# Kernel tuning notes

Measured on AMD Instinct MI355X. Metric: run time of the kernel, lower is better.

Reference implementation:

```python
import jax, jax.numpy as jnp
import numpy as np

B = 8192          # tokens
H = 7168          # hidden size
E = 256           # routed experts
N_GROUP = 8
GROUP_SIZE = 32   # E // N_GROUP
TOPK_GROUP = 4
TOPK = 8
SCALE = 2.5
EPS = 1e-20
NEG_INF = -jnp.inf


def setup_inputs() -> dict:
    key = jax.random.key(0)
    k1, k2, k3 = jax.random.split(key, 3)
    x = jax.random.normal(k1, (1, 1, B, H), dtype=jnp.float32)
    weight = jax.random.normal(k2, (H, E), dtype=jnp.float32) * 0.02
    bias = jax.random.uniform(k3, (E,), dtype=jnp.float32)  # e_score_correction_bias
    return {"x": x, "weight": weight, "bias": bias}


def reference(x, weight, bias):
    # gate projection + softmax over experts
    logits = jnp.einsum('abth,he->abte', x, weight)          # [1,1,B,E]
    scores = jax.nn.softmax(logits, axis=-1)                 # [1,1,B,E]
    scores_with_bias = scores + bias                         # bias-corrected scores

    # group-limited routing: top-2 per group, summed -> group score
    grouped = scores_with_bias.reshape(1, 1, B, N_GROUP, GROUP_SIZE)
    top2_vals, _ = jax.lax.top_k(grouped, 2)                 # [1,1,B,8,2]
    group_scores = top2_vals.sum(axis=-1)                    # [1,1,B,8]

    # select top-4 groups, build {1, -inf} mask over groups
    _, top4_idx = jax.lax.top_k(group_scores, TOPK_GROUP)    # [1,1,B,4]
    sel = jax.nn.one_hot(top4_idx, N_GROUP, dtype=scores.dtype).sum(axis=-2)  # [1,1,B,8]
    group_mask = jnp.where(sel > 0, 1.0, NEG_INF)
    expert_mask = jnp.repeat(group_mask, GROUP_SIZE, axis=-1)  # [1,1,B,256]

    # mask (multiplicative, as in original), top-8 experts
    masked = scores_with_bias * expert_mask
    _, top8_idx = jax.lax.top_k(masked, TOPK)                # [1,1,B,8]

    # gather unbiased scores, normalize, eps + scale
    w = jnp.take_along_axis(scores, top8_idx, axis=-1)       # [1,1,B,8]
    w = w / w.sum(axis=-1, keepdims=True)
    w = (w + EPS) * SCALE
    return w, top8_idx
```

## Files before the change

### kernel.cpp

```cpp
#include <hip/hip_runtime.h>
#include <math.h>

#define B_TOK 8192
#define H_DIM 7168
#define E_NUM 256
#define NKS   4
#define KSL   (H_DIM / NKS)
#define BK    32
#define NSTEP (KSL / BK)
#define BM    128
#define NMT   (B_TOK / BM)
#define FLAG_CAP 512
#define TAU   2e-6

typedef _Float16 f16;
typedef __attribute__((ext_vector_type(8))) _Float16 f16x8;
typedef __attribute__((ext_vector_type(4))) float    f32x4;

typedef __attribute__((address_space(1))) const void gvoid_t;
typedef __attribute__((address_space(3))) void       lvoid_t;

__device__ inline void gload_lds16(const void* g, void* s) {
    __builtin_amdgcn_global_load_lds((gvoid_t*)g, (lvoid_t*)s, 16, 0, 0);
}

__device__ __forceinline__ void route_token(
    const double* lv, const double* bj, int l, int hf, int t,
    float* __restrict__ out, double* ming_adj, double* ming_grp)
{
    double m = fmax(fmax(lv[0], lv[1]), fmax(lv[2], lv[3]));
    #pragma unroll
    for (int d = 1; d < 64; d <<= 1) m = fmax(m, __shfl_xor(m, d, 64));
    double sc[4], zs = 0.0;
    #pragma unroll
    for (int q = 0; q < 4; ++q) { sc[q] = exp(lv[q] - m); zs += sc[q]; }
    #pragma unroll
    for (int d = 1; d < 64; d <<= 1) zs += __shfl_xor(zs, d, 64);
    double swb[4];
    #pragma unroll
    for (int q = 0; q < 4; ++q) { sc[q] /= zs; swb[q] = sc[q] + bj[q]; }

    double gsq[4];
    #pragma unroll
    for (int q = 0; q < 4; ++q) {
        double a = swb[q], b = -INFINITY;
        #pragma unroll
        for (int d = 1; d <= 16; d <<= 1) {
            double oa = __shfl_xor(a, d, 64), ob = __shfl_xor(b, d, 64);
            double na = fmax(a, oa);
            double nb = fmax(fmin(a, oa), fmax(b, ob));
            a = na; b = nb;
        }
        gsq[q] = a + b;
    }
    double gsv[8];
    #pragma unroll
    for (int q = 0; q < 4; ++q) {
        gsv[2 * q]     = __shfl(gsq[q], 0, 64);
        gsv[2 * q + 1] = __shfl(gsq[q], 32, 64);
    }

    unsigned selmask = 0; double g4 = 0.0, g5 = 0.0;
    #pragma unroll
    for (int k = 0; k < 5; ++k) {
        double best = -INFINITY; int bg = 0;
        #pragma unroll
        for (int g = 0; g < 8; ++g)
            if (gsv[g] > best) { best = gsv[g]; bg = g; }
        if (k < 4) { selmask |= 1u << bg; g4 = best; } else g5 = best;
        #pragma unroll
        for (int g = 0; g < 8; ++g) if (g == bg) gsv[g] = -INFINITY;
    }
    *ming_grp = g4 - g5;

    double mk[4];
    #pragma unroll
    for (int q = 0; q < 4; ++q)
        mk[q] = ((selmask >> (2 * q + hf)) & 1u) ? swb[q] : -INFINITY;

    double wk[8]; int ek[8]; double wsum = 0.0;
    double prev = 0.0, ming = 1e300;
    #pragma unroll
    for (int k = 0; k < 9; ++k) {
        double vbest = mk[0]; int ebest = l;
        #pragma unroll
        for (int q = 1; q < 4; ++q)
            if (mk[q] > vbest) { vbest = mk[q]; ebest = l + 64 * q; }
        #pragma unroll
        for (int d = 1; d < 64; d <<= 1) {
            double ov = __shfl_xor(vbest, d, 64);
            int    oe = __shfl_xor(ebest, d, 64);
            if (ov > vbest || (ov == vbest && oe < ebest)) { vbest = ov; ebest = oe; }
        }
        if (k > 0) ming = fmin(ming, prev - vbest);
        prev = vbest;
        if (k < 8) {
            const int ol = ebest & 63, oq = ebest >> 6;
            if (l == ol) {
                #pragma unroll
                for (int q = 0; q < 4; ++q) if (q == oq) mk[q] = -INFINITY;
            }
            double cand = (oq == 0) ? sc[0] : (oq == 1) ? sc[1] : (oq == 2) ? sc[2] : sc[3];
            double sv = __shfl(cand, ol, 64);
            wk[k] = sv; ek[k] = ebest; wsum += sv;
        }
    }
    *ming_adj = ming;

    if (l == 0) {
        const double inv = 1.0 / wsum;
        #pragma unroll
        for (int k = 0; k < 8; ++k) {
            out[(size_t)t * 8 + k] = (float)((wk[k] * inv + 1e-20) * 2.5);
            out[(size_t)B_TOK * 8 + (size_t)t * 8 + k] = (float)ek[k];
        }
    }
}

__global__ void convert_w_kernel(const float* __restrict__ W,
                                 f16* __restrict__ wpk,
                                 unsigned* __restrict__ flags) {
    if (blockIdx.x == 0 && threadIdx.x == 0) flags[0] = 0;
    int g = blockIdx.x * 256 + threadIdx.x;
    int n = g & 255, k = g >> 8;
    float v = W[(size_t)k * E_NUM + n];
    f16 hi = (f16)v;
    f16 lo = (f16)(v - (float)hi);
    int kf = k >> 5, tq = (k >> 3) & 3, j = k & 7;
    int nf = n >> 4, l = tq * 16 + (n & 15);
    size_t off = ((size_t)(kf * 16 + nf) * 2) * 512 + (size_t)l * 8 + j;
    wpk[off]       = hi;
    wpk[off + 512] = lo;
}

__global__ __launch_bounds__(512, 1)
void gemm_kernel(const float* __restrict__ x,
                 const f16* __restrict__ wpk,
                 float* __restrict__ partial) {
    __shared__ __align__(16) char lds[2][49152];

    const int tid = threadIdx.x;
    const int l   = tid & 63;
    const int wid = tid >> 6;
    const int mt  = blockIdx.x >> 2;
    const int ks  = blockIdx.x & 3;
    const int wr  = wid >> 2;
    const int wc  = wid & 3;

    const int row = mt * BM + wid * 16 + (l & 15);
    const float* xrow = x + (size_t)row * H_DIM + ks * KSL + (l >> 4) * 8;

    f32x4 acc[4][4];
    #pragma unroll
    for (int mi = 0; mi < 4; ++mi)
        #pragma unroll
        for (int ni = 0; ni < 4; ++ni) acc[mi][ni] = (f32x4)0.0f;

    {
        float4 a0 = *reinterpret_cast<const float4*>(xrow);
        float4 a1 = *reinterpret_cast<const float4*>(xrow + 4);
        const int kf = ks * NSTEP + 0;
        #pragma unroll
        for (int i = 0; i < 4; ++i) {
            int fi = wid * 4 + i, nf = fi >> 1, h = fi & 1;
            const f16* src = wpk + ((size_t)(kf * 16 + nf) * 2 + h) * 512 + (size_t)l * 8;
            gload_lds16(src, &lds[0][16384 + (nf * 2 + h) * 1024]);
        }
        float fv[8] = {a0.x, a0.y, a0.z, a0.w, a1.x, a1.y, a1.z, a1.w};
        f16x8 hv, lo;
        #pragma unroll
        for (int j = 0; j < 8; ++j) {
            f16 hh = (f16)fv[j];
            hv[j] = hh;
            lo[j] = (f16)(fv[j] - (float)hh);
        }
        *reinterpret_cast<f16x8*>(&lds[0][(wid * 2 + 0) * 1024 + l * 16]) = hv;
        *reinterpret_cast<f16x8*>(&lds[0][(wid * 2 + 1) * 1024 + l * 16]) = lo;
        __syncthreads();
    }

    int cur = 0;
    for (int s = 0; s < NSTEP; ++s) {
        const bool hn = (s + 1) < NSTEP;
        const int  sn = hn ? s + 1 : s;

        float4 a0 = *reinterpret_cast<const float4*>(xrow + (size_t)sn * BK);
        float4 a1 = *reinterpret_cast<const float4*>(xrow + (size_t)sn * BK + 4);

        if (hn) {
            const int kf = ks * NSTEP + sn;
            char* nb = lds[cur ^ 1];
            #pragma unroll
            for (int i = 0; i < 4; ++i) {
                int fi = wid * 4 + i, nf = fi >> 1, h = fi & 1;
                const f16* src = wpk + ((size_t)(kf * 16 + nf) * 2 + h) * 512 + (size_t)l * 8;
                gload_lds16(src, &nb[16384 + (nf * 2 + h) * 1024]);
            }
        }

        const char* Ab = lds[cur];
        const char* Bb = lds[cur] + 16384;
        f16x8 af[4][2], bf[4][2];
        #pragma unroll
        for (int mi = 0; mi < 4; ++mi)
            #pragma unroll
            for (int h = 0; h < 2; ++h)
                af[mi][h] = *reinterpret_cast<const f16x8*>(
                    Ab + ((wr * 4 + mi) * 2 + h) * 1024 + l * 16);
        #pragma unroll
        for (int ni = 0; ni < 4; ++ni)
            #pragma unroll
            for (int h = 0; h < 2; ++h)
                bf[ni][h] = *reinterpret_cast<const f16x8*>(
                    Bb + ((wc * 4 + ni) * 2 + h) * 1024 + l * 16);
        #pragma unroll
        for (int mi = 0; mi < 4; ++mi)
            #pragma unroll
            for (int ni = 0; ni < 4; ++ni) {
                acc[mi][ni] = __builtin_amdgcn_mfma_f32_16x16x32_f16(
                    af[mi][0], bf[ni][0], acc[mi][ni], 0, 0, 0);
                acc[mi][ni] = __builtin_amdgcn_mfma_f32_16x16x32_f16(
                    af[mi][0], bf[ni][1], acc[mi][ni], 0, 0, 0);
                acc[mi][ni] = __builtin_amdgcn_mfma_f32_16x16x32_f16(
                    af[mi][1], bf[ni][0], acc[mi][ni], 0, 0, 0);
            }

        if (hn) {
            char* nb = lds[cur ^ 1];
            float fv[8] = {a0.x, a0.y, a0.z, a0.w, a1.x, a1.y, a1.z, a1.w};
            f16x8 hv, lo;
            #pragma unroll
            for (int j = 0; j < 8; ++j) {
                f16 hh = (f16)fv[j];
                hv[j] = hh;
                lo[j] = (f16)(fv[j] - (float)hh);
            }
            *reinterpret_cast<f16x8*>(&nb[(wid * 2 + 0) * 1024 + l * 16]) = hv;
            *reinterpret_cast<f16x8*>(&nb[(wid * 2 + 1) * 1024 + l * 16]) = lo;
        }
        __syncthreads();
        cur ^= 1;
    }

    float* pbase = partial + ((size_t)ks * B_TOK + (size_t)mt * BM) * E_NUM;
    #pragma unroll
    for (int mi = 0; mi < 4; ++mi)
        #pragma unroll
        for (int ni = 0; ni < 4; ++ni)
            #pragma unroll
            for (int r = 0; r < 4; ++r) {
                int rr = wr * 64 + mi * 16 + (l >> 4) * 4 + r;
                int cc = wc * 64 + ni * 16 + (l & 15);
                pbase[(size_t)rr * E_NUM + cc] = acc[mi][ni][r];
            }
}

__global__ __launch_bounds__(512, 1)
void routing_kernel(const float* __restrict__ partial,
                    const float* __restrict__ bias,
                    float* __restrict__ out,
                    unsigned* __restrict__ flags) {
    const int tid  = threadIdx.x;
    const int l    = tid & 63;
    const int wv   = tid >> 6;
    const int tok0 = blockIdx.x * 32;

    double bj[4];
    #pragma unroll
    for (int q = 0; q < 4; ++q) bj[q] = (double)bias[l + 64 * q];
    const int hf = l >> 5;

    for (int i = 0; i < 4; ++i) {
        const int t = tok0 + wv * 4 + i;
        double lv[4];
        #pragma unroll
        for (int q = 0; q < 4; ++q) {
            double s = 0.0;
            #pragma unroll
            for (int ksl = 0; ksl < NKS; ++ksl)
                s += (double)partial[((size_t)ksl * B_TOK + t) * E_NUM + l + 64 * q];
            lv[q] = s;
        }
        double ma, mg;
        route_token(lv, bj, l, hf, t, out, &ma, &mg);
        if (l == 0 && (ma < TAU || mg < TAU)) {
            unsigned idx = atomicAdd(&flags[0], 1u);
            if (idx < FLAG_CAP) flags[1 + idx] = (unsigned)t;
        }
    }
}

__global__ __launch_bounds__(256)
void recompute_dot_kernel(const float* __restrict__ x,
                          const float* __restrict__ W,
                          const unsigned* __restrict__ flags,
                          double* __restrict__ dpart) {
    __shared__ float xs[896];
    unsigned count = flags[0]; if (count > FLAG_CAP) count = FLAG_CAP;
    unsigned nj = count * 8;
    for (unsigned j = blockIdx.x; j < nj; j += gridDim.x) {
        unsigned li = j >> 3, sl = j & 7;
        int t = (int)flags[1 + li];
        const float* xb = x + (size_t)t * H_DIM + sl * 896;
        for (int i = threadIdx.x; i < 224; i += 256)
            *reinterpret_cast<float4*>(&xs[i * 4]) =
                *reinterpret_cast<const float4*>(xb + i * 4);
        __syncthreads();
        const float* wp = W + (size_t)(sl * 896) * E_NUM + threadIdx.x;
        double acc = 0.0;
        #pragma unroll 8
        for (int k = 0; k < 896; ++k)
            acc += (double)xs[k] * (double)wp[(size_t)k * E_NUM];
        dpart[((size_t)li * 8 + sl) * E_NUM + threadIdx.x] = acc;
        __syncthreads();
    }
}

__global__ __launch_bounds__(64)
void recompute_route_kernel(const double* __restrict__ dpart,
                            const float* __restrict__ bias,
                            const unsigned* __restrict__ flags,
                            float* __restrict__ out) {
    const int l = threadIdx.x;
    unsigned count = flags[0]; if (count > FLAG_CAP) count = FLAG_CAP;
    double bj[4];
    #pragma unroll
    for (int q = 0; q < 4; ++q) bj[q] = (double)bias[l + 64 * q];
    const int hf = l >> 5;
    for (unsigned li = blockIdx.x; li < count; li += gridDim.x) {
        int t = (int)flags[1 + li];
        double lv[4];
        #pragma unroll
        for (int q = 0; q < 4; ++q) {
            double s = 0.0;
            #pragma unroll
            for (int sl = 0; sl < 8; ++sl)
                s += dpart[((size_t)li * 8 + sl) * E_NUM + l + 64 * q];
            lv[q] = s;
        }
        double ma, mg;
        route_token(lv, bj, l, hf, t, out, &ma, &mg);
    }
}

#define TM 32
#define HB 64
#define FNST (H_DIM / HB)

__global__ __launch_bounds__(512, 1)
void moe_gate_fallback(const float* __restrict__ x,
                       const float* __restrict__ W,
                       const float* __restrict__ bias,
                       float* __restrict__ out) {
    __shared__ double xs[TM][HB];
    const int tid  = threadIdx.x;
    const int l    = tid & 63;
    const int wv   = tid >> 6;
    const int tok0 = blockIdx.x * TM;
    const int tl = tid >> 4;
    const int ho = (tid & 15) * 4;

    double acc[4][4];
    #pragma unroll
    for (int i = 0; i < 4; ++i)
        #pragma unroll
        for (int q = 0; q < 4; ++q) acc[i][q] = 0.0;

    const float* xrow = x + (size_t)(tok0 + tl) * H_DIM + ho;
    float4 v = *reinterpret_cast<const float4*>(xrow);

    for (int s = 0; s < FNST; ++s) {
        __syncthreads();
        xs[tl][ho + 0] = (double)v.x;
        xs[tl][ho + 1] = (double)v.y;
        xs[tl][ho + 2] = (double)v.z;
        xs[tl][ho + 3] = (double)v.w;
        __syncthreads();
        const int sn = (s + 1 < FNST) ? s + 1 : s;
        v = *reinterpret_cast<const float4*>(xrow + (size_t)sn * HB);
        const float* wh = W + (size_t)s * HB * E_NUM + l;
        #pragma unroll 4
        for (int h = 0; h < HB; h += 2) {
            float wf0[4], wf1[4];
            #pragma unroll
            for (int q = 0; q < 4; ++q) {
                wf0[q] = wh[(size_t)h       * E_NUM + q * 64];
                wf1[q] = wh[(size_t)(h + 1) * E_NUM + q * 64];
            }
            #pragma unroll
            for (int i = 0; i < 4; ++i) {
                const double2 xv = *reinterpret_cast<const double2*>(&xs[wv * 4 + i][h]);
                #pragma unroll
                for (int q = 0; q < 4; ++q) {
                    acc[i][q] = fma((double)wf0[q], xv.x, acc[i][q]);
                    acc[i][q] = fma((double)wf1[q], xv.y, acc[i][q]);
                }
            }
        }
    }

    double bj[4];
    #pragma unroll
    for (int q = 0; q < 4; ++q) bj[q] = (double)bias[l + 64 * q];
    const int hf = l >> 5;

    for (int i = 0; i < 4; ++i) {
        const int t = tok0 + wv * 4 + i;
        double lv[4];
        #pragma unroll
        for (int q = 0; q < 4; ++q) lv[q] = acc[i][q];
        double ma, mg;
        route_token(lv, bj, l, hf, t, out, &ma, &mg);
    }
}

extern "C" void kernel_launch(void* const* d_in, const int* in_sizes, int n_in,
                              void* d_out, int out_size, void* d_ws, size_t ws_size,
                              hipStream_t stream) {
    const float* x    = (const float*)d_in[0];
    const float* W    = (const float*)d_in[1];
    const float* bias = (const float*)d_in[2];
    float* out = (float*)d_out;

    const size_t flag_off = 7864320;
    const size_t part_off = 8u * 1024 * 1024;
    const size_t need     = part_off + (size_t)NKS * B_TOK * E_NUM * 4;

    if (ws_size >= need) {
        f16*      wpk     = (f16*)d_ws;
        unsigned* flags   = (unsigned*)((char*)d_ws + flag_off);
        float*    partial = (float*)((char*)d_ws + part_off);
        double*   dpart   = (double*)((char*)d_ws + part_off);

        convert_w_kernel<<<(H_DIM * E_NUM) / 256, 256, 0, stream>>>(W, wpk, flags);
        gemm_kernel<<<NMT * NKS, 512, 0, stream>>>(x, wpk, partial);
        routing_kernel<<<B_TOK / 32, 512, 0, stream>>>(partial, bias, out, flags);
        recompute_dot_kernel<<<1024, 256, 0, stream>>>(x, W, flags, dpart);
        recompute_route_kernel<<<64, 64, 0, stream>>>(dpart, bias, flags, out);
    } else {
        moe_gate_fallback<<<B_TOK / 32, 512, 0, stream>>>(x, W, bias, out);
    }
}
```

Baseline: 216.4 us.

## Triple-buffer GEMM LDS with explicit waitcnt pipeline, block swizzle, and MFMA priority

Moves the gate GEMM from a double-buffered LDS loop to a three-buffer pipeline, unrolled by two steps. Weight tiles are staged two steps ahead and x loads are prefetched into registers, with explicit vmcnt/lgkmcnt waits and raw s_barrier in place of __syncthreads. The block index is swizzled so that concurrently running blocks share the same K-slice, and s_setprio raises wave priority around the MFMA section. The cost is 144KB of LDS per block, plus waitcnt counts that depend on the exact number of outstanding loads, which is fragile.

After: 213.1 us. No clear change (-1.5%).

```diff
diff --git a/kernel.cpp b/kernel.cpp
--- a/kernel.cpp
+++ b/kernel.cpp
@@ -23,6 +23,11 @@
 __device__ inline void gload_lds16(const void* g, void* s) {
     __builtin_amdgcn_global_load_lds((gvoid_t*)g, (lvoid_t*)s, 16, 0, 0);
 }
+
+#define WAITVM(N) do { asm volatile("s_waitcnt vmcnt(" #N ")" ::: "memory"); \
+                       __builtin_amdgcn_sched_barrier(0); } while (0)
+#define WAITLGKM0() do { asm volatile("s_waitcnt lgkmcnt(0)" ::: "memory"); \
+                       __builtin_amdgcn_sched_barrier(0); } while (0)
 
 __device__ __forceinline__ void route_token(
     const double* lv, const double* bj, int l, int hf, int t,
@@ -133,22 +138,81 @@
     wpk[off + 512] = lo;
 }
 
+__device__ __forceinline__ void stage_B(const f16* __restrict__ wpk, int kf,
+                                        char* bbuf, int wid, int l) {
+    #pragma unroll
+    for (int i = 0; i < 4; ++i) {
+        int fi = wid * 4 + i, nf = fi >> 1, h = fi & 1;
+        const f16* src = wpk + ((size_t)(kf * 16 + nf) * 2 + h) * 512 + (size_t)l * 8;
+        gload_lds16(src, bbuf + 16384 + (nf * 2 + h) * 1024);
+    }
+}
+
+__device__ __forceinline__ void write_A(char* buf, int wid, int l,
+                                        float4 a0, float4 a1) {
+    float fv[8] = {a0.x, a0.y, a0.z, a0.w, a1.x, a1.y, a1.z, a1.w};
+    f16x8 hv, lo;
+    #pragma unroll
+    for (int j = 0; j < 8; ++j) {
+        f16 hh = (f16)fv[j];
+        hv[j] = hh;
+        lo[j] = (f16)(fv[j] - (float)hh);
+    }
+    *reinterpret_cast<f16x8*>(&buf[(wid * 2 + 0) * 1024 + l * 16]) = hv;
+    *reinterpret_cast<f16x8*>(&buf[(wid * 2 + 1) * 1024 + l * 16]) = lo;
+}
+
+__device__ __forceinline__ void compute_step(const char* buf, int wr, int wc,
+                                             int l, f32x4 (&acc)[4][4]) {
+    const char* Ab = buf;
+    const char* Bb = buf + 16384;
+    f16x8 af[4][2], bf[4][2];
+    #pragma unroll
+    for (int mi = 0; mi < 4; ++mi)
+        #pragma unroll
+        for (int h = 0; h < 2; ++h)
+            af[mi][h] = *reinterpret_cast<const f16x8*>(
+                Ab + ((wr * 4 + mi) * 2 + h) * 1024 + l * 16);
+    #pragma unroll
+    for (int ni = 0; ni < 4; ++ni)
+        #pragma unroll
+        for (int h = 0; h < 2; ++h)
+            bf[ni][h] = *reinterpret_cast<const f16x8*>(
+                Bb + ((wc * 4 + ni) * 2 + h) * 1024 + l * 16);
+    __builtin_amdgcn_s_setprio(1);
+    #pragma unroll
+    for (int mi = 0; mi < 4; ++mi)
+        #pragma unroll
+        for (int ni = 0; ni < 4; ++ni) {
+            acc[mi][ni] = __builtin_amdgcn_mfma_f32_16x16x32_f16(
+                af[mi][0], bf[ni][0], acc[mi][ni], 0, 0, 0);
+            acc[mi][ni] = __builtin_amdgcn_mfma_f32_16x16x32_f16(
+                af[mi][0], bf[ni][1], acc[mi][ni], 0, 0, 0);
+            acc[mi][ni] = __builtin_amdgcn_mfma_f32_16x16x32_f16(
+                af[mi][1], bf[ni][0], acc[mi][ni], 0, 0, 0);
+        }
+    __builtin_amdgcn_s_setprio(0);
+}
+
 __global__ __launch_bounds__(512, 1)
 void gemm_kernel(const float* __restrict__ x,
                  const f16* __restrict__ wpk,
                  float* __restrict__ partial) {
-    __shared__ __align__(16) char lds[2][49152];
+    __shared__ __align__(16) char lds[3][49152];
 
     const int tid = threadIdx.x;
     const int l   = tid & 63;
     const int wid = tid >> 6;
-    const int mt  = blockIdx.x >> 2;
-    const int ks  = blockIdx.x & 3;
+    const int bid = blockIdx.x;
+    const int swz = (bid & 7) * 32 + (bid >> 3);
+    const int ks  = swz >> 6;
+    const int mt  = swz & 63;
     const int wr  = wid >> 2;
     const int wc  = wid & 3;
 
     const int row = mt * BM + wid * 16 + (l & 15);
     const float* xrow = x + (size_t)row * H_DIM + ks * KSL + (l >> 4) * 8;
+    const int kf0 = ks * NSTEP;
 
     f32x4 acc[4][4];
     #pragma unroll
@@ -156,90 +220,54 @@
         #pragma unroll
         for (int ni = 0; ni < 4; ++ni) acc[mi][ni] = (f32x4)0.0f;
 
+    float4 pf0e, pf1e, pf0o, pf1o;
+
     {
-        float4 a0 = *reinterpret_cast<const float4*>(xrow);
-        float4 a1 = *reinterpret_cast<const float4*>(xrow + 4);
-        const int kf = ks * NSTEP + 0;
-        #pragma unroll
-        for (int i = 0; i < 4; ++i) {
-            int fi = wid * 4 + i, nf = fi >> 1, h = fi & 1;
-            const f16* src = wpk + ((size_t)(kf * 16 + nf) * 2 + h) * 512 + (size_t)l * 8;
-            gload_lds16(src, &lds[0][16384 + (nf * 2 + h) * 1024]);
-        }
-        float fv[8] = {a0.x, a0.y, a0.z, a0.w, a1.x, a1.y, a1.z, a1.w};
-        f16x8 hv, lo;
-        #pragma unroll
-        for (int j = 0; j < 8; ++j) {
-            f16 hh = (f16)fv[j];
-            hv[j] = hh;
-            lo[j] = (f16)(fv[j] - (float)hh);
-        }
-        *reinterpret_cast<f16x8*>(&lds[0][(wid * 2 + 0) * 1024 + l * 16]) = hv;
-        *reinterpret_cast<f16x8*>(&lds[0][(wid * 2 + 1) * 1024 + l * 16]) = lo;
-        __syncthreads();
+        float4 a00 = *reinterpret_cast<const float4*>(xrow);
+        float4 a01 = *reinterpret_cast<const float4*>(xrow + 4);
+        pf0o = *reinterpret_cast<const float4*>(xrow + BK);
+        pf1o = *reinterpret_cast<const float4*>(xrow + BK + 4);
+        stage_B(wpk, kf0 + 0, lds[0], wid, l);
+        stage_B(wpk, kf0 + 1, lds[1], wid, l);
+        write_A(lds[0], wid, l, a00, a01);
+        asm volatile("s_waitcnt vmcnt(0) lgkmcnt(0)" ::: "memory");
+        __builtin_amdgcn_sched_barrier(0);
+        __builtin_amdgcn_s_barrier();
     }
 
     int cur = 0;
-    for (int s = 0; s < NSTEP; ++s) {
-        const bool hn = (s + 1) < NSTEP;
-        const int  sn = hn ? s + 1 : s;
-
-        float4 a0 = *reinterpret_cast<const float4*>(xrow + (size_t)sn * BK);
-        float4 a1 = *reinterpret_cast<const float4*>(xrow + (size_t)sn * BK + 4);
-
-        if (hn) {
-            const int kf = ks * NSTEP + sn;
-            char* nb = lds[cur ^ 1];
-            #pragma unroll
-            for (int i = 0; i < 4; ++i) {
-                int fi = wid * 4 + i, nf = fi >> 1, h = fi & 1;
-                const f16* src = wpk + ((size_t)(kf * 16 + nf) * 2 + h) * 512 + (size_t)l * 8;
-                gload_lds16(src, &nb[16384 + (nf * 2 + h) * 1024]);
-            }
-        }
-
-        const char* Ab = lds[cur];
-        const char* Bb = lds[cur] + 16384;
-        f16x8 af[4][2], bf[4][2];
-        #pragma unroll
-        for (int mi = 0; mi < 4; ++mi)
-            #pragma unroll
-            for (int h = 0; h < 2; ++h)
-                af[mi][h] = *reinterpret_cast<const f16x8*>(
-                    Ab + ((wr * 4 + mi) * 2 + h) * 1024 + l * 16);
-        #pragma unroll
-        for (int ni = 0; ni < 4; ++ni)
-            #pragma unroll
-            for (int h = 0; h < 2; ++h)
-                bf[ni][h] = *reinterpret_cast<const f16x8*>(
-                    Bb + ((wc * 4 + ni) * 2 + h) * 1024 + l * 16);
-        #pragma unroll
-        for (int mi = 0; mi < 4; ++mi)
-            #pragma unroll
-            for (int ni = 0; ni < 4; ++ni) {
-                acc[mi][ni] = __builtin_amdgcn_mfma_f32_16x16x32_f16(
-                    af[mi][0], bf[ni][0], acc[mi][ni], 0, 0, 0);
-                acc[mi][ni] = __builtin_amdgcn_mfma_f32_16x16x32_f16(
-                    af[mi][0], bf[ni][1], acc[mi][ni], 0, 0, 0);
-                acc[mi][ni] = __builtin_amdgcn_mfma_f32_16x16x32_f16(
-                    af[mi][1], bf[ni][0], acc[mi][ni], 0, 0, 0);
-            }
-
-        if (hn) {
-            char* nb = lds[cur ^ 1];
-            float fv[8] = {a0.x, a0.y, a0.z, a0.w, a1.x, a1.y, a1.z, a1.w};
-            f16x8 hv, lo;
-            #pragma unroll
-            for (int j = 0; j < 8; ++j) {
-                f16 hh = (f16)fv[j];
-                hv[j] = hh;
-                lo[j] = (f16)(fv[j] - (float)hh);
-            }
-            *reinterpret_cast<f16x8*>(&nb[(wid * 2 + 0) * 1024 + l * 16]) = hv;
-            *reinterpret_cast<f16x8*>(&nb[(wid * 2 + 1) * 1024 + l * 16]) = lo;
-        }
-        __syncthreads();
-        cur ^= 1;
+    for (int t = 0; t < NSTEP; t += 2) {
+        int nx1 = cur + 1; if (nx1 == 3) nx1 = 0;
+        int nx2 = nx1 + 1; if (nx2 == 3) nx2 = 0;
+
+        if (t + 2 < NSTEP) {
+            pf0e = *reinterpret_cast<const float4*>(xrow + (size_t)(t + 2) * BK);
+            pf1e = *reinterpret_cast<const float4*>(xrow + (size_t)(t + 2) * BK + 4);
+            stage_B(wpk, kf0 + t + 2, lds[nx2], wid, l);
+            WAITVM(12);
+        } else {
+            WAITVM(6);
+        }
+        compute_step(lds[cur], wr, wc, l, acc);
+        write_A(lds[nx1], wid, l, pf0o, pf1o);
+        WAITLGKM0();
+        __builtin_amdgcn_s_barrier();
+
+        if (t + 3 < NSTEP) {
+            pf0o = *reinterpret_cast<const float4*>(xrow + (size_t)(t + 3) * BK);
+            pf1o = *reinterpret_cast<const float4*>(xrow + (size_t)(t + 3) * BK + 4);
+            stage_B(wpk, kf0 + t + 3, lds[cur], wid, l);
+            WAITVM(12);
+        } else {
+            WAITVM(0);
+        }
+        compute_step(lds[nx1], wr, wc, l, acc);
+        if (t + 2 < NSTEP)
+            write_A(lds[nx2], wid, l, pf0e, pf1e);
+        WAITLGKM0();
+        __builtin_amdgcn_s_barrier();
+
+        cur = nx2;
     }
 
     float* pbase = partial + ((size_t)ks * B_TOK + (size_t)mt * BM) * E_NUM;
```

## Replace LDS-staged GEMM with direct register loads and software pipelining

Applied to the files above, without the earlier changes.

The GEMM no longer stages A and B tiles through shared memory with barriers. Each wave loads its x rows and pre-packed weight fragments straight from global memory into registers, double-buffered across even and odd k-steps, and uses setprio around the MFMA bursts. Block indices are also swizzled so that blocks sharing a k-slice of weights run together. This removes LDS traffic and __syncthreads, but each wave now reloads x rows that other waves in the same row group also fetch, and register pressure rises.

Result: slower. 302.1 us (+39.6%).

```diff
diff --git a/kernel.cpp b/kernel.cpp
--- a/kernel.cpp
+++ b/kernel.cpp
@@ -16,13 +16,6 @@
 typedef _Float16 f16;
 typedef __attribute__((ext_vector_type(8))) _Float16 f16x8;
 typedef __attribute__((ext_vector_type(4))) float    f32x4;
-
-typedef __attribute__((address_space(1))) const void gvoid_t;
-typedef __attribute__((address_space(3))) void       lvoid_t;
-
-__device__ inline void gload_lds16(const void* g, void* s) {
-    __builtin_amdgcn_global_load_lds((gvoid_t*)g, (lvoid_t*)s, 16, 0, 0);
-}
 
 __device__ __forceinline__ void route_token(
     const double* lv, const double* bj, int l, int hf, int t,
@@ -133,22 +126,64 @@
     wpk[off + 512] = lo;
 }
 
+__device__ __forceinline__ void load_A(const float* const (&xb)[4], int t,
+                                       float4 (&raw)[4][2], int mf) {
+    raw[mf][0] = *reinterpret_cast<const float4*>(xb[mf] + (size_t)t * BK);
+    raw[mf][1] = *reinterpret_cast<const float4*>(xb[mf] + (size_t)t * BK + 4);
+}
+
+__device__ __forceinline__ void load_B(const f16* wb, int t, f16x8 (&b)[4][2]) {
+    const f16* p = wb + (size_t)t * 16384;
+    #pragma unroll
+    for (int i = 0; i < 4; ++i)
+        #pragma unroll
+        for (int h = 0; h < 2; ++h)
+            b[i][h] = *reinterpret_cast<const f16x8*>(p + i * 1024 + h * 512);
+}
+
+__device__ __forceinline__ void conv_mfma(const float4 (&raw)[4][2],
+                                          const f16x8 (&b)[4][2],
+                                          f32x4 (&acc)[4][4], int mf) {
+    float fv[8] = {raw[mf][0].x, raw[mf][0].y, raw[mf][0].z, raw[mf][0].w,
+                   raw[mf][1].x, raw[mf][1].y, raw[mf][1].z, raw[mf][1].w};
+    f16x8 ah, al;
+    #pragma unroll
+    for (int j = 0; j < 8; ++j) {
+        f16 hh = (f16)fv[j];
+        ah[j] = hh;
+        al[j] = (f16)(fv[j] - (float)hh);
+    }
+    __builtin_amdgcn_s_setprio(1);
+    #pragma unroll
+    for (int ni = 0; ni < 4; ++ni) {
+        acc[mf][ni] = __builtin_amdgcn_mfma_f32_16x16x32_f16(ah, b[ni][0], acc[mf][ni], 0, 0, 0);
+        acc[mf][ni] = __builtin_amdgcn_mfma_f32_16x16x32_f16(ah, b[ni][1], acc[mf][ni], 0, 0, 0);
+        acc[mf][ni] = __builtin_amdgcn_mfma_f32_16x16x32_f16(al, b[ni][0], acc[mf][ni], 0, 0, 0);
+    }
+    __builtin_amdgcn_s_setprio(0);
+}
+
 __global__ __launch_bounds__(512, 1)
 void gemm_kernel(const float* __restrict__ x,
                  const f16* __restrict__ wpk,
                  float* __restrict__ partial) {
-    __shared__ __align__(16) char lds[2][49152];
-
     const int tid = threadIdx.x;
     const int l   = tid & 63;
     const int wid = tid >> 6;
-    const int mt  = blockIdx.x >> 2;
-    const int ks  = blockIdx.x & 3;
+    const int bid = blockIdx.x;
+    const int swz = (bid & 7) * 32 + (bid >> 3);
+    const int ks  = swz >> 6;
+    const int mt  = swz & 63;
     const int wr  = wid >> 2;
     const int wc  = wid & 3;
 
-    const int row = mt * BM + wid * 16 + (l & 15);
-    const float* xrow = x + (size_t)row * H_DIM + ks * KSL + (l >> 4) * 8;
+    const float* xb[4];
+    #pragma unroll
+    for (int mf = 0; mf < 4; ++mf) {
+        int row = mt * BM + wr * 64 + mf * 16 + (l & 15);
+        xb[mf] = x + (size_t)row * H_DIM + ks * KSL + (l >> 4) * 8;
+    }
+    const f16* wb = wpk + ((size_t)(ks * NSTEP) * 16 + wc * 4) * 2 * 512 + (size_t)l * 8;
 
     f32x4 acc[4][4];
     #pragma unroll
@@ -156,90 +191,35 @@
         #pragma unroll
         for (int ni = 0; ni < 4; ++ni) acc[mi][ni] = (f32x4)0.0f;
 
-    {
-        float4 a0 = *reinterpret_cast<const float4*>(xrow);
-        float4 a1 = *reinterpret_cast<const float4*>(xrow + 4);
-        const int kf = ks * NSTEP + 0;
-        #pragma unroll
-        for (int i = 0; i < 4; ++i) {
-            int fi = wid * 4 + i, nf = fi >> 1, h = fi & 1;
-            const f16* src = wpk + ((size_t)(kf * 16 + nf) * 2 + h) * 512 + (size_t)l * 8;
-            gload_lds16(src, &lds[0][16384 + (nf * 2 + h) * 1024]);
-        }
-        float fv[8] = {a0.x, a0.y, a0.z, a0.w, a1.x, a1.y, a1.z, a1.w};
-        f16x8 hv, lo;
-        #pragma unroll
-        for (int j = 0; j < 8; ++j) {
-            f16 hh = (f16)fv[j];
-            hv[j] = hh;
-            lo[j] = (f16)(fv[j] - (float)hh);
-        }
-        *reinterpret_cast<f16x8*>(&lds[0][(wid * 2 + 0) * 1024 + l * 16]) = hv;
-        *reinterpret_cast<f16x8*>(&lds[0][(wid * 2 + 1) * 1024 + l * 16]) = lo;
-        __syncthreads();
-    }
-
-    int cur = 0;
-    for (int s = 0; s < NSTEP; ++s) {
-        const bool hn = (s + 1) < NSTEP;
-        const int  sn = hn ? s + 1 : s;
-
-        float4 a0 = *reinterpret_cast<const float4*>(xrow + (size_t)sn * BK);
-        float4 a1 = *reinterpret_cast<const float4*>(xrow + (size_t)sn * BK + 4);
-
-        if (hn) {
-            const int kf = ks * NSTEP + sn;
-            char* nb = lds[cur ^ 1];
-            #pragma unroll
-            for (int i = 0; i < 4; ++i) {
-                int fi = wid * 4 + i, nf = fi >> 1, h = fi & 1;
-                const f16* src = wpk + ((size_t)(kf * 16 + nf) * 2 + h) * 512 + (size_t)l * 8;
-                gload_lds16(src, &nb[16384 + (nf * 2 + h) * 1024]);
-            }
-        }
-
-        const char* Ab = lds[cur];
-        const char* Bb = lds[cur] + 16384;
-        f16x8 af[4][2], bf[4][2];
-        #pragma unroll
-        for (int mi = 0; mi < 4; ++mi)
-            #pragma unroll
-            for (int h = 0; h < 2; ++h)
-                af[mi][h] = *reinterpret_cast<const f16x8*>(
-                    Ab + ((wr * 4 + mi) * 2 + h) * 1024 + l * 16);
-        #pragma unroll
-        for (int ni = 0; ni < 4; ++ni)
-            #pragma unroll
-            for (int h = 0; h < 2; ++h)
-                bf[ni][h] = *reinterpret_cast<const f16x8*>(
-                    Bb + ((wc * 4 + ni) * 2 + h) * 1024 + l * 16);
-        #pragma unroll
-        for (int mi = 0; mi < 4; ++mi)
-            #pragma unroll
-            for (int ni = 0; ni < 4; ++ni) {
-                acc[mi][ni] = __builtin_amdgcn_mfma_f32_16x16x32_f16(
-                    af[mi][0], bf[ni][0], acc[mi][ni], 0, 0, 0);
-                acc[mi][ni] = __builtin_amdgcn_mfma_f32_16x16x32_f16(
-                    af[mi][0], bf[ni][1], acc[mi][ni], 0, 0, 0);
-                acc[mi][ni] = __builtin_amdgcn_mfma_f32_16x16x32_f16(
-                    af[mi][1], bf[ni][0], acc[mi][ni], 0, 0, 0);
-            }
-
-        if (hn) {
-            char* nb = lds[cur ^ 1];
-            float fv[8] = {a0.x, a0.y, a0.z, a0.w, a1.x, a1.y, a1.z, a1.w};
-            f16x8 hv, lo;
-            #pragma unroll
-            for (int j = 0; j < 8; ++j) {
-                f16 hh = (f16)fv[j];
-                hv[j] = hh;
-                lo[j] = (f16)(fv[j] - (float)hh);
-            }
-            *reinterpret_cast<f16x8*>(&nb[(wid * 2 + 0) * 1024 + l * 16]) = hv;
-            *reinterpret_cast<f16x8*>(&nb[(wid * 2 + 1) * 1024 + l * 16]) = lo;
-        }
-        __syncthreads();
-        cur ^= 1;
+    float4 rawE[4][2], rawO[4][2];
+    f16x8  bE[4][2],   bO[4][2];
+
+    #pragma unroll
+    for (int mf = 0; mf < 4; ++mf) load_A(xb, 0, rawE, mf);
+    load_B(wb, 0, bE);
+    #pragma unroll
+    for (int mf = 0; mf < 4; ++mf) load_A(xb, 1, rawO, mf);
+    load_B(wb, 1, bO);
+
+    for (int t = 0; t < NSTEP; t += 2) {
+        {
+            const int sn = (t + 2 < NSTEP) ? t + 2 : NSTEP - 1;
+            #pragma unroll
+            for (int mf = 0; mf < 4; ++mf) {
+                conv_mfma(rawE, bE, acc, mf);
+                load_A(xb, sn, rawE, mf);
+            }
+            load_B(wb, sn, bE);
+        }
+        {
+            const int sn = (t + 3 < NSTEP) ? t + 3 : NSTEP - 1;
+            #pragma unroll
+            for (int mf = 0; mf < 4; ++mf) {
+                conv_mfma(rawO, bO, acc, mf);
+                load_A(xb, sn, rawO, mf);
+            }
+            load_B(wb, sn, bO);
+        }
     }
 
     float* pbase = partial + ((size_t)ks * B_TOK + (size_t)mt * BM) * E_NUM;
```

## Single-buffer LDS, double split-K, and raise GEMM occupancy to four blocks per CU

Applied to the files above, without the earlier changes.

The gate GEMM now splits K eight ways instead of four, which doubles the block count. It uses a single 48KB LDS buffer instead of a double buffer, and launch bounds now request four 512-thread blocks per CU. Latency hiding moves from intra-block double buffering to inter-block occupancy, and x loads are register-prefetched two steps ahead. This requires two barriers per step, doubles the partial-sum traffic to the routing kernel, and may force register spilling with the 64 accumulator registers under the tighter bound.

Measured after the change: 236.6 us. 1.09x slower.

```diff
diff --git a/kernel.cpp b/kernel.cpp
--- a/kernel.cpp
+++ b/kernel.cpp
@@ -4,7 +4,7 @@
 #define B_TOK 8192
 #define H_DIM 7168
 #define E_NUM 256
-#define NKS   4
+#define NKS   8
 #define KSL   (H_DIM / NKS)
 #define BK    32
 #define NSTEP (KSL / BK)
@@ -128,27 +128,83 @@
     f16 lo = (f16)(v - (float)hi);
     int kf = k >> 5, tq = (k >> 3) & 3, j = k & 7;
     int nf = n >> 4, l = tq * 16 + (n & 15);
-    size_t off = ((size_t)(kf * 16 + nf) * 2) * 512 + (size_t)l * 8 + j;
+    size_t off = ((size_t)(kf * 32 + nf * 2)) * 512 + (size_t)l * 8 + j;
     wpk[off]       = hi;
     wpk[off + 512] = lo;
 }
 
-__global__ __launch_bounds__(512, 1)
+__device__ __forceinline__ void stage_B(const f16* __restrict__ wb, int kf,
+                                        char* lds, int wid, int l) {
+    #pragma unroll
+    for (int i = 0; i < 4; ++i) {
+        int fi = wid * 4 + i;
+        gload_lds16(wb + ((size_t)kf * 32 + fi) * 512 + (size_t)l * 8,
+                    lds + 16384 + fi * 1024);
+    }
+}
+
+__device__ __forceinline__ void write_A(char* lds, int wid, int l,
+                                        float4 a0, float4 a1) {
+    float fv[8] = {a0.x, a0.y, a0.z, a0.w, a1.x, a1.y, a1.z, a1.w};
+    f16x8 hv, lo;
+    #pragma unroll
+    for (int j = 0; j < 8; ++j) {
+        f16 hh = (f16)fv[j];
+        hv[j] = hh;
+        lo[j] = (f16)(fv[j] - (float)hh);
+    }
+    *reinterpret_cast<f16x8*>(&lds[(wid * 2 + 0) * 1024 + l * 16]) = hv;
+    *reinterpret_cast<f16x8*>(&lds[(wid * 2 + 1) * 1024 + l * 16]) = lo;
+}
+
+__device__ __forceinline__ void compute_step(const char* lds, int wr, int wc,
+                                             int l, f32x4 (&acc)[4][4]) {
+    const char* Ab = lds;
+    const char* Bb = lds + 16384;
+    f16x8 af[4][2], bf[4][2];
+    #pragma unroll
+    for (int mi = 0; mi < 4; ++mi)
+        #pragma unroll
+        for (int h = 0; h < 2; ++h)
+            af[mi][h] = *reinterpret_cast<const f16x8*>(
+                Ab + ((wr * 4 + mi) * 2 + h) * 1024 + l * 16);
+    #pragma unroll
+    for (int ni = 0; ni < 4; ++ni)
+        #pragma unroll
+        for (int h = 0; h < 2; ++h)
+            bf[ni][h] = *reinterpret_cast<const f16x8*>(
+                Bb + ((wc * 4 + ni) * 2 + h) * 1024 + l * 16);
+    #pragma unroll
+    for (int mi = 0; mi < 4; ++mi)
+        #pragma unroll
+        for (int ni = 0; ni < 4; ++ni) {
+            acc[mi][ni] = __builtin_amdgcn_mfma_f32_16x16x32_f16(
+                af[mi][0], bf[ni][0], acc[mi][ni], 0, 0, 0);
+            acc[mi][ni] = __builtin_amdgcn_mfma_f32_16x16x32_f16(
+                af[mi][0], bf[ni][1], acc[mi][ni], 0, 0, 0);
+            acc[mi][ni] = __builtin_amdgcn_mfma_f32_16x16x32_f16(
+                af[mi][1], bf[ni][0], acc[mi][ni], 0, 0, 0);
+        }
+}
+
+__global__ __launch_bounds__(512, 4)
 void gemm_kernel(const float* __restrict__ x,
                  const f16* __restrict__ wpk,
                  float* __restrict__ partial) {
-    __shared__ __align__(16) char lds[2][49152];
+    __shared__ __align__(16) char lds[49152];
 
     const int tid = threadIdx.x;
     const int l   = tid & 63;
     const int wid = tid >> 6;
-    const int mt  = blockIdx.x >> 2;
-    const int ks  = blockIdx.x & 3;
+    const int bid = blockIdx.x;
+    const int ks  = bid & 7;
+    const int mt  = bid >> 3;
     const int wr  = wid >> 2;
     const int wc  = wid & 3;
 
     const int row = mt * BM + wid * 16 + (l & 15);
     const float* xrow = x + (size_t)row * H_DIM + ks * KSL + (l >> 4) * 8;
+    const f16* wb = wpk + (size_t)ks * NSTEP * 32 * 512;
 
     f32x4 acc[4][4];
     #pragma unroll
@@ -156,90 +212,28 @@
         #pragma unroll
         for (int ni = 0; ni < 4; ++ni) acc[mi][ni] = (f32x4)0.0f;
 
-    {
-        float4 a0 = *reinterpret_cast<const float4*>(xrow);
-        float4 a1 = *reinterpret_cast<const float4*>(xrow + 4);
-        const int kf = ks * NSTEP + 0;
-        #pragma unroll
-        for (int i = 0; i < 4; ++i) {
-            int fi = wid * 4 + i, nf = fi >> 1, h = fi & 1;
-            const f16* src = wpk + ((size_t)(kf * 16 + nf) * 2 + h) * 512 + (size_t)l * 8;
-            gload_lds16(src, &lds[0][16384 + (nf * 2 + h) * 1024]);
-        }
-        float fv[8] = {a0.x, a0.y, a0.z, a0.w, a1.x, a1.y, a1.z, a1.w};
-        f16x8 hv, lo;
-        #pragma unroll
-        for (int j = 0; j < 8; ++j) {
-            f16 hh = (f16)fv[j];
-            hv[j] = hh;
-            lo[j] = (f16)(fv[j] - (float)hh);
-        }
-        *reinterpret_cast<f16x8*>(&lds[0][(wid * 2 + 0) * 1024 + l * 16]) = hv;
-        *reinterpret_cast<f16x8*>(&lds[0][(wid * 2 + 1) * 1024 + l * 16]) = lo;
+    float4 a0 = *reinterpret_cast<const float4*>(xrow);
+    float4 a1 = *reinterpret_cast<const float4*>(xrow + 4);
+    stage_B(wb, 0, lds, wid, l);
+    write_A(lds, wid, l, a0, a1);
+    a0 = *reinterpret_cast<const float4*>(xrow + BK);
+    a1 = *reinterpret_cast<const float4*>(xrow + BK + 4);
+    __syncthreads();
+
+    for (int t = 0; t < NSTEP; ++t) {
+        float4 a0n, a1n;
+        if (t + 2 < NSTEP) {
+            a0n = *reinterpret_cast<const float4*>(xrow + (size_t)(t + 2) * BK);
+            a1n = *reinterpret_cast<const float4*>(xrow + (size_t)(t + 2) * BK + 4);
+        }
+        compute_step(lds, wr, wc, l, acc);
         __syncthreads();
-    }
-
-    int cur = 0;
-    for (int s = 0; s < NSTEP; ++s) {
-        const bool hn = (s + 1) < NSTEP;
-        const int  sn = hn ? s + 1 : s;
-
-        float4 a0 = *reinterpret_cast<const float4*>(xrow + (size_t)sn * BK);
-        float4 a1 = *reinterpret_cast<const float4*>(xrow + (size_t)sn * BK + 4);
-
-        if (hn) {
-            const int kf = ks * NSTEP + sn;
-            char* nb = lds[cur ^ 1];
-            #pragma unroll
-            for (int i = 0; i < 4; ++i) {
-                int fi = wid * 4 + i, nf = fi >> 1, h = fi & 1;
-                const f16* src = wpk + ((size_t)(kf * 16 + nf) * 2 + h) * 512 + (size_t)l * 8;
-                gload_lds16(src, &nb[16384 + (nf * 2 + h) * 1024]);
-            }
-        }
-
-        const char* Ab = lds[cur];
-        const char* Bb = lds[cur] + 16384;
-        f16x8 af[4][2], bf[4][2];
-        #pragma unroll
-        for (int mi = 0; mi < 4; ++mi)
-            #pragma unroll
-            for (int h = 0; h < 2; ++h)
-                af[mi][h] = *reinterpret_cast<const f16x8*>(
-                    Ab + ((wr * 4 + mi) * 2 + h) * 1024 + l * 16);
-        #pragma unroll
-        for (int ni = 0; ni < 4; ++ni)
-            #pragma unroll
-            for (int h = 0; h < 2; ++h)
-                bf[ni][h] = *reinterpret_cast<const f16x8*>(
-                    Bb + ((wc * 4 + ni) * 2 + h) * 1024 + l * 16);
-        #pragma unroll
-        for (int mi = 0; mi < 4; ++mi)
-            #pragma unroll
-            for (int ni = 0; ni < 4; ++ni) {
-                acc[mi][ni] = __builtin_amdgcn_mfma_f32_16x16x32_f16(
-                    af[mi][0], bf[ni][0], acc[mi][ni], 0, 0, 0);
-                acc[mi][ni] = __builtin_amdgcn_mfma_f32_16x16x32_f16(
-                    af[mi][0], bf[ni][1], acc[mi][ni], 0, 0, 0);
-                acc[mi][ni] = __builtin_amdgcn_mfma_f32_16x16x32_f16(
-                    af[mi][1], bf[ni][0], acc[mi][ni], 0, 0, 0);
-            }
-
-        if (hn) {
-            char* nb = lds[cur ^ 1];
-            float fv[8] = {a0.x, a0.y, a0.z, a0.w, a1.x, a1.y, a1.z, a1.w};
-            f16x8 hv, lo;
-            #pragma unroll
-            for (int j = 0; j < 8; ++j) {
-                f16 hh = (f16)fv[j];
-                hv[j] = hh;
-                lo[j] = (f16)(fv[j] - (float)hh);
-            }
-            *reinterpret_cast<f16x8*>(&nb[(wid * 2 + 0) * 1024 + l * 16]) = hv;
-            *reinterpret_cast<f16x8*>(&nb[(wid * 2 + 1) * 1024 + l * 16]) = lo;
-        }
-        __syncthreads();
-        cur ^= 1;
+        if (t + 1 < NSTEP) {
+            stage_B(wb, t + 1, lds, wid, l);
+            write_A(lds, wid, l, a0, a1);
+            a0 = a0n; a1 = a1n;
+            __syncthreads();
+        }
     }
 
     float* pbase = partial + ((size_t)ks * B_TOK + (size_t)mt * BM) * E_NUM;
```
